# Kernel tuning notes

Hardware: AMD Instinct MI355X
Metric: run time of the kernel (lower is better)

## Reference

```python
import jax, jax.numpy as jnp
import numpy as np

N_NODES = 10000
N_EDGES = 160000
N_GRAPHS = 64
X_IN = 128
HID = 64
EDGE_DIM = 16
HEADS = 4
# (in_dim, out_dim_per_head) for the 3 TransformerConv layers (concat=False)
DIMS = [(X_IN, HID), (HID, 2 * HID), (2 * HID, HID)]
WNAMES = [f"{n}{l}" for l in (1, 2, 3) for n in ("wq", "bq", "wk", "bk", "wv", "bv", "we", "ws", "bs")]


def setup_inputs() -> dict:
    key = jax.random.key(0)
    ks = iter(jax.random.split(key, 64))
    inp = {}
    inp["x"] = jax.random.normal(next(ks), (N_NODES, X_IN), jnp.float32)
    inp["edge_index"] = jax.random.randint(next(ks), (2, N_EDGES), 0, N_NODES)
    inp["edge_attr"] = jax.random.normal(next(ks), (N_EDGES, EDGE_DIM), jnp.float32)
    inp["batch"] = jnp.sort(jax.random.randint(next(ks), (N_NODES,), 0, N_GRAPHS))
    for l, (din, dout) in enumerate(DIMS, 1):
        hd = HEADS * dout
        for nm, shape in [("wq", (din, hd)), ("wk", (din, hd)), ("wv", (din, hd)),
                          ("we", (EDGE_DIM, hd)), ("ws", (din, dout))]:
            inp[f"{nm}{l}"] = jax.random.normal(next(ks), shape, jnp.float32) * 0.05
        inp[f"bq{l}"] = jnp.zeros((hd,), jnp.float32)
        inp[f"bk{l}"] = jnp.zeros((hd,), jnp.float32)
        inp[f"bv{l}"] = jnp.zeros((hd,), jnp.float32)
        inp[f"bs{l}"] = jnp.zeros((dout,), jnp.float32)
    return inp


def _transformer_conv(x, src, dst, edge_attr, wq, bq, wk, bk, wv, bv, we, ws, bs, dout):
    """PyG TransformerConv, concat=False, root_weight=True, with edge features."""
    N = x.shape[0]
    q = (x @ wq + bq).reshape(N, HEADS, dout)
    k = (x @ wk + bk).reshape(N, HEADS, dout)
    v = (x @ wv + bv).reshape(N, HEADS, dout)
    e = (edge_attr @ we).reshape(-1, HEADS, dout)  # [E, H, C]
    k_j = k[src] + e                               # edge-conditioned keys
    alpha = jnp.einsum("ehd,ehd->eh", q[dst], k_j) * (1.0 / float(dout) ** 0.5)  # [E, H]
    # numerically stable segment softmax over incoming edges of each dst node
    a_max = jax.ops.segment_max(alpha, dst, num_segments=N)
    ex = jnp.exp(alpha - a_max[dst])
    den = jax.ops.segment_sum(ex, dst, num_segments=N)
    attn = ex / den[dst]
    agg = jax.ops.segment_sum((v[src] + e) * attn[..., None], dst, num_segments=N)  # [N, H, C]
    return agg.mean(axis=1) + x @ ws + bs  # concat=False -> head mean; + skip


def _forward(x, edge_attr, edge_index, batch, params):
    src, dst = edge_index[0], edge_index[1]
    h = x
    for l, (_, dout) in enumerate(DIMS, 1):
        p = [params[f"{n}{l}"] for n in ("wq", "bq", "wk", "bk", "wv", "bv", "we", "ws", "bs")]
        h = jax.nn.elu(_transformer_conv(h, src, dst, edge_attr, *p, dout))
    # global mean pool over graphs
    s = jax.ops.segment_sum(h, batch, num_segments=N_GRAPHS)
    cnt = jax.ops.segment_sum(jnp.ones((h.shape[0], 1), h.dtype), batch, num_segments=N_GRAPHS)
    return s / jnp.maximum(cnt, 1.0)


def reference(x, edge_index, edge_attr, batch,
              wq1, bq1, wk1, bk1, wv1, bv1, we1, ws1, bs1,
              wq2, bq2, wk2, bk2, wv2, bv2, we2, ws2, bs2,
              wq3, bq3, wk3, bk3, wv3, bv3, we3, ws3, bs3):
    params = dict(locals())
    return _forward(x, edge_attr, edge_index, batch, params)
```

## Files before the change

### kernel.cpp

```cpp
#include <hip/hip_runtime.h>
#include <hip/hip_fp16.h>
#include <math.h>

#define N_NODES 10000
#define N_EDGES 160000
#define N_GRAPHS 64

using half8 = __attribute__((ext_vector_type(8))) _Float16;
using floatx4 = __attribute__((ext_vector_type(4))) float;

template <int K, int HD, int DOUT>
__global__ __launch_bounds__(256) void gemm_mfma(
    const __half* __restrict__ A, const __half* __restrict__ Wp,
    const float* __restrict__ bias, float* __restrict__ QS,
    __half* __restrict__ KV, int M) {
  constexpr int QSS = HD + DOUT;
  constexpr int KS = K / 32;
  const int tid = threadIdx.x;
  const int wave = tid >> 6, lane = tid & 63;
  const int quad = lane >> 4, n16 = lane & 15;
  const int row0 = blockIdx.y * 64 + wave * 16;
  const int col0 = blockIdx.x * 64;
  const int nblk0 = blockIdx.x * 4;

  const int arow = min(row0 + n16, M - 1);
  half8 afrag[KS];
#pragma unroll
  for (int s = 0; s < KS; ++s)
    afrag[s] = *reinterpret_cast<const half8*>(A + (size_t)arow * K + s * 32 + quad * 8);

  floatx4 acc[4];
#pragma unroll
  for (int t = 0; t < 4; ++t) {
    acc[t] = (floatx4){0.f, 0.f, 0.f, 0.f};
#pragma unroll
    for (int s = 0; s < KS; ++s) {
      half8 bf = *reinterpret_cast<const half8*>(
          Wp + (((size_t)(nblk0 + t) * KS + s) * 64 + lane) * 8);
      acc[t] = __builtin_amdgcn_mfma_f32_16x16x32_f16(afrag[s], bf, acc[t], 0, 0, 0);
    }
  }

#pragma unroll
  for (int t = 0; t < 4; ++t) {
    const int c = col0 + t * 16 + n16;
    const float bv = bias[c];
#pragma unroll
    for (int r = 0; r < 4; ++r) {
      int row = row0 + quad * 4 + r;
      if (row < M) {
        float val = acc[t][r] + bv;
        if (c < HD)
          QS[(size_t)row * QSS + c] = val;
        else if (c < 3 * HD)
          KV[(size_t)row * (2 * HD) + (c - HD)] = __float2half(val);
        else
          QS[(size_t)row * QSS + HD + (c - 3 * HD)] = val;
      }
    }
  }
}

__device__ inline void pack_layer(int i, int K, int HD, int DOUT,
                                  const float* wq, const float* wk,
                                  const float* wv, const float* wsk,
                                  const float* bq, const float* bk,
                                  const float* bv, const float* bs,
                                  __half* Wp, float* bcat) {
  const int W = 3 * HD + DOUT;
  const int KS = K / 32;
  if (i < K * W) {
    int j = i & 7, lane = (i >> 3) & 63, fs = i >> 9;
    int nblk = fs / KS, s = fs - nblk * KS;
    int quad = lane >> 4, n = lane & 15;
    int k = s * 32 + quad * 8 + j, c = nblk * 16 + n;
    float v;
    if (c < HD)           v = wq[k * HD + c];
    else if (c < 2 * HD)  v = wk[k * HD + (c - HD)];
    else if (c < 3 * HD)  v = wv[k * HD + (c - 2 * HD)];
    else                  v = wsk[k * DOUT + (c - 3 * HD)];
    Wp[i] = __float2half(v);
  } else {
    int c = i - K * W;
    float v;
    if (c < HD)           v = bq[c];
    else if (c < 2 * HD)  v = bk[c - HD];
    else if (c < 3 * HD)  v = bv[c - 2 * HD];
    else                  v = bs[c - 3 * HD];
    bcat[c] = v;
  }
}

#define T1 107328
#define T2 215488
#define T3 322816

__global__ void pack_all(
    const float* wq1, const float* wk1, const float* wv1, const float* ws1,
    const float* bq1, const float* bk1, const float* bv1, const float* bs1,
    const float* wq2, const float* wk2, const float* wv2, const float* ws2,
    const float* bq2, const float* bk2, const float* bv2, const float* bs2,
    const float* wq3, const float* wk3, const float* wv3, const float* ws3,
    const float* bq3, const float* bk3, const float* bv3, const float* bs3,
    __half* W1, float* b1, __half* W2, float* b2, __half* W3, float* b3) {
  for (int i = blockIdx.x * blockDim.x + threadIdx.x; i < T3;
       i += gridDim.x * blockDim.x) {
    if (i < T1)
      pack_layer(i, 128, 256, 64, wq1, wk1, wv1, ws1, bq1, bk1, bv1, bs1, W1, b1);
    else if (i < T2)
      pack_layer(i - T1, 64, 512, 128, wq2, wk2, wv2, ws2, bq2, bk2, bv2, bs2, W2, b2);
    else
      pack_layer(i - T2, 128, 256, 64, wq3, wk3, wv3, ws3, bq3, bk3, bv3, bs3, W3, b3);
  }
}

__global__ void conv_f16(const float* __restrict__ in, __half* __restrict__ out,
                         int n4) {
  int i = blockIdx.x * blockDim.x + threadIdx.x;
  if (i < n4) {
    float4 v = reinterpret_cast<const float4*>(in)[i];
    __half2* o = reinterpret_cast<__half2*>(out) + 2 * i;
    o[0] = __floats2half2_rn(v.x, v.y);
    o[1] = __floats2half2_rn(v.z, v.w);
  }
}

__global__ void zero_ints(int* __restrict__ a, int n) {
  for (int i = blockIdx.x * blockDim.x + threadIdx.x; i < n;
       i += gridDim.x * blockDim.x) a[i] = 0;
}

__global__ void count_dst(const int* __restrict__ dst, int* __restrict__ cnt) {
  int e = blockIdx.x * blockDim.x + threadIdx.x;
  if (e < N_EDGES) atomicAdd(&cnt[dst[e]], 1);
}

__global__ __launch_bounds__(256) void scan_offs(const int* __restrict__ cnt,
                                                 int* __restrict__ offs) {
  __shared__ int part[256];
  const int t = threadIdx.x;
  const int chunk = (N_NODES + 255) / 256;
  const int b = t * chunk;
  const int e = min(N_NODES, b + chunk);
  int s = 0;
  for (int i = b; i < e; ++i) s += cnt[i];
  part[t] = s;
  __syncthreads();
  for (int off = 1; off < 256; off <<= 1) {
    int v = (t >= off) ? part[t - off] : 0;
    __syncthreads();
    part[t] += v;
    __syncthreads();
  }
  int pre = (t == 0) ? 0 : part[t - 1];
  for (int i = b; i < e; ++i) { offs[i] = pre; pre += cnt[i]; }
  if (t == 0) offs[N_NODES] = part[255];
}

__global__ void scatter_csr(const int* __restrict__ src, const int* __restrict__ dst,
                            const float* __restrict__ edge_attr,
                            const int* __restrict__ offs, int* __restrict__ cursor,
                            int* __restrict__ csr_src, float* __restrict__ csr_ea) {
  int e = blockIdx.x * blockDim.x + threadIdx.x;
  if (e < N_EDGES) {
    int d = dst[e];
    int pos = offs[d] + atomicAdd(&cursor[d], 1);
    csr_src[pos] = src[e];
    float4* o4 = reinterpret_cast<float4*>(csr_ea + (size_t)pos * 16);
    const float4* s4 = reinterpret_cast<const float4*>(edge_attr + (size_t)e * 16);
    o4[0] = s4[0]; o4[1] = s4[1]; o4[2] = s4[2]; o4[3] = s4[3];
  }
}

template <int NV>
__device__ inline void load_kv(const __half* p, float4 (&dst)[NV]) {
  if (NV == 1) {
    float2 r = *reinterpret_cast<const float2*>(p);
    const __half2* h = reinterpret_cast<const __half2*>(&r);
    float2 a = __half22float2(h[0]), b = __half22float2(h[1]);
    dst[0] = make_float4(a.x, a.y, b.x, b.y);
  } else {
    float4 r = *reinterpret_cast<const float4*>(p);
    const __half2* h = reinterpret_cast<const __half2*>(&r);
    float2 a = __half22float2(h[0]), b = __half22float2(h[1]);
    float2 c = __half22float2(h[2]), d = __half22float2(h[3]);
    dst[0] = make_float4(a.x, a.y, b.x, b.y);
    dst[NV - 1] = make_float4(c.x, c.y, d.x, d.y);
  }
}

template <int DOUT>
__global__ __launch_bounds__(256) void edge_attn(
    const float* __restrict__ QS, const __half* __restrict__ KV,
    const float* __restrict__ we, const int* __restrict__ csr_src,
    const float* __restrict__ csr_ea, const int* __restrict__ offs,
    float* __restrict__ out, __half* __restrict__ out16) {
  constexpr int HD = 4 * DOUT;
  constexpr int QSS = HD + DOUT;
  constexpr int KVS = 2 * HD;
  constexpr int NV = DOUT / 64;
  const float SCALE = (DOUT == 64) ? 0.125f : 0.08838834764831845f;

  const int lane = threadIdx.x & 63;
  const int h = lane >> 4, t16 = lane & 15;
  const int n = blockIdx.x * 4 + (threadIdx.x >> 6);
  const int c0 = t16 * 4 * NV;

  const float* base = QS + (size_t)n * QSS;
  float4 q[NV], acc[NV];
#pragma unroll
  for (int v = 0; v < NV; ++v) {
    float4 qq = *reinterpret_cast<const float4*>(base + h * DOUT + c0 + 4 * v);
    qq.x *= SCALE; qq.y *= SCALE; qq.z *= SCALE; qq.w *= SCALE;
    q[v] = qq;
    acc[v] = make_float4(0.f, 0.f, 0.f, 0.f);
  }

  float g = 0.f;
#pragma unroll
  for (int d = 0; d < 16; ++d) {
    float p = 0.f;
    const float* wb = we + d * HD + h * DOUT + c0;
#pragma unroll
    for (int v = 0; v < NV; ++v) {
      float4 w4 = *reinterpret_cast<const float4*>(wb + 4 * v);
      p += q[v].x * w4.x + q[v].y * w4.y + q[v].z * w4.z + q[v].w * w4.w;
    }
    p += __shfl_xor(p, 1);
    p += __shfl_xor(p, 2);
    p += __shfl_xor(p, 4);
    p += __shfl_xor(p, 8);
    if (t16 == d) g = p;
  }

  float m = -1e30f, lsum = 0.f, tacc = 0.f;

  const int s0 = offs[n], s1 = offs[n + 1];
  int ii = s0;

  for (; ii + 4 <= s1; ii += 4) {
    int sj[4];
#pragma unroll
    for (int j = 0; j < 4; ++j) sj[j] = csr_src[ii + j];
    float ea[4];
#pragma unroll
    for (int j = 0; j < 4; ++j) ea[j] = csr_ea[(size_t)(ii + j) * 16 + t16];
    float4 kj[4][NV], vj[4][NV];
#pragma unroll
    for (int j = 0; j < 4; ++j) {
      const __half* rb = KV + (size_t)sj[j] * KVS + h * DOUT + c0;
      load_kv<NV>(rb, kj[j]);
      load_kv<NV>(rb + HD, vj[j]);
    }
    float a[4];
#pragma unroll
    for (int j = 0; j < 4; ++j) {
      float p = ea[j] * g;
#pragma unroll
      for (int v = 0; v < NV; ++v)
        p += q[v].x * kj[j][v].x + q[v].y * kj[j][v].y + q[v].z * kj[j][v].z +
             q[v].w * kj[j][v].w;
      a[j] = p;
    }
#pragma unroll
    for (int j = 0; j < 4; ++j) {
      a[j] += __shfl_xor(a[j], 1);
      a[j] += __shfl_xor(a[j], 2);
      a[j] += __shfl_xor(a[j], 4);
      a[j] += __shfl_xor(a[j], 8);
    }
    float mn = fmaxf(fmaxf(fmaxf(a[0], a[1]), fmaxf(a[2], a[3])), m);
    float fac = __expf(m - mn);
    float p0 = __expf(a[0] - mn), p1 = __expf(a[1] - mn);
    float p2 = __expf(a[2] - mn), p3 = __expf(a[3] - mn);
    m = mn;
    lsum = lsum * fac + (p0 + p1 + p2 + p3);
    tacc = tacc * fac + p0 * ea[0] + p1 * ea[1] + p2 * ea[2] + p3 * ea[3];
#pragma unroll
    for (int v = 0; v < NV; ++v) {
      float4 av = acc[v];
      av.x = av.x * fac + p0 * vj[0][v].x + p1 * vj[1][v].x + p2 * vj[2][v].x + p3 * vj[3][v].x;
      av.y = av.y * fac + p0 * vj[0][v].y + p1 * vj[1][v].y + p2 * vj[2][v].y + p3 * vj[3][v].y;
      av.z = av.z * fac + p0 * vj[0][v].z + p1 * vj[1][v].z + p2 * vj[2][v].z + p3 * vj[3][v].z;
      av.w = av.w * fac + p0 * vj[0][v].w + p1 * vj[1][v].w + p2 * vj[2][v].w + p3 * vj[3][v].w;
      acc[v] = av;
    }
  }

  for (; ii < s1; ++ii) {
    int s = csr_src[ii];
    float ea0 = csr_ea[(size_t)ii * 16 + t16];
    const __half* rb = KV + (size_t)s * KVS + h * DOUT + c0;
    float4 kk[NV], vv[NV];
    load_kv<NV>(rb, kk);
    load_kv<NV>(rb + HD, vv);
    float a = ea0 * g;
#pragma unroll
    for (int v = 0; v < NV; ++v)
      a += q[v].x * kk[v].x + q[v].y * kk[v].y + q[v].z * kk[v].z + q[v].w * kk[v].w;
    a += __shfl_xor(a, 1);
    a += __shfl_xor(a, 2);
    a += __shfl_xor(a, 4);
    a += __shfl_xor(a, 8);
    float mn = fmaxf(m, a);
    float fac = __expf(m - mn);
    float p = __expf(a - mn);
    m = mn;
    lsum = lsum * fac + p;
    tacc = tacc * fac + p * ea0;
#pragma unroll
    for (int v = 0; v < NV; ++v) {
      acc[v].x = acc[v].x * fac + p * vv[v].x;
      acc[v].y = acc[v].y * fac + p * vv[v].y;
      acc[v].z = acc[v].z * fac + p * vv[v].z;
      acc[v].w = acc[v].w * fac + p * vv[v].w;
    }
  }

  float invl = (lsum > 0.f) ? 1.f / lsum : 0.f;
  float tn = tacc * invl;
  float4 val[NV];
#pragma unroll
  for (int v = 0; v < NV; ++v) {
    val[v].x = acc[v].x * invl; val[v].y = acc[v].y * invl;
    val[v].z = acc[v].z * invl; val[v].w = acc[v].w * invl;
  }
#pragma unroll
  for (int d = 0; d < 16; ++d) {
    float td = __shfl(tn, (lane & 48) | d);
    const float* wb = we + d * HD + h * DOUT + c0;
#pragma unroll
    for (int v = 0; v < NV; ++v) {
      float4 w4 = *reinterpret_cast<const float4*>(wb + 4 * v);
      val[v].x += td * w4.x; val[v].y += td * w4.y;
      val[v].z += td * w4.z; val[v].w += td * w4.w;
    }
  }
#pragma unroll
  for (int v = 0; v < NV; ++v) {
    val[v].x += __shfl_xor(val[v].x, 16); val[v].x += __shfl_xor(val[v].x, 32);
    val[v].y += __shfl_xor(val[v].y, 16); val[v].y += __shfl_xor(val[v].y, 32);
    val[v].z += __shfl_xor(val[v].z, 16); val[v].z += __shfl_xor(val[v].z, 32);
    val[v].w += __shfl_xor(val[v].w, 16); val[v].w += __shfl_xor(val[v].w, 32);
  }
  if (h == 0) {
#pragma unroll
    for (int v = 0; v < NV; ++v) {
      float4 sk = *reinterpret_cast<const float4*>(base + HD + c0 + 4 * v);
      float4 o;
      o.x = 0.25f * val[v].x + sk.x;
      o.y = 0.25f * val[v].y + sk.y;
      o.z = 0.25f * val[v].z + sk.z;
      o.w = 0.25f * val[v].w + sk.w;
      o.x = (o.x > 0.f) ? o.x : expm1f(o.x);
      o.y = (o.y > 0.f) ? o.y : expm1f(o.y);
      o.z = (o.z > 0.f) ? o.z : expm1f(o.z);
      o.w = (o.w > 0.f) ? o.w : expm1f(o.w);
      *reinterpret_cast<float4*>(out + (size_t)n * DOUT + c0 + 4 * v) = o;
      __half2* o16 = reinterpret_cast<__half2*>(out16 + (size_t)n * DOUT + c0 + 4 * v);
      o16[0] = __floats2half2_rn(o.x, o.y);
      o16[1] = __floats2half2_rn(o.z, o.w);
    }
  }
}

__device__ inline int lower_bound(const int* b, int n, int v) {
  int lo = 0, hi = n;
  while (lo < hi) {
    int mid = (lo + hi) >> 1;
    if (b[mid] < v) lo = mid + 1; else hi = mid;
  }
  return lo;
}

__global__ __launch_bounds__(256) void pool_all(const float* __restrict__ h,
                                                const int* __restrict__ batch,
                                                float* __restrict__ out) {
  const int g = blockIdx.x;
  const int start = lower_bound(batch, N_NODES, g);
  const int end = lower_bound(batch, N_NODES, g + 1);
  const int c = threadIdx.x & 63, j = threadIdx.x >> 6;
  float s = 0.f;
  for (int n = start + j; n < end; n += 4) s += h[(size_t)n * 64 + c];
  __shared__ float red[4][64];
  red[j][c] = s;
  __syncthreads();
  if (j == 0) {
    float tot = red[0][c] + red[1][c] + red[2][c] + red[3][c];
    out[g * 64 + c] = tot / (float)max(end - start, 1);
  }
}

extern "C" void kernel_launch(void* const* d_in, const int* in_sizes, int n_in,
                              void* d_out, int out_size, void* d_ws, size_t ws_size,
                              hipStream_t stream) {
  const float* x = (const float*)d_in[0];
  const int* edge_index = (const int*)d_in[1];
  const float* edge_attr = (const float*)d_in[2];
  const int* batch = (const int*)d_in[3];
  const int* srcp = edge_index;
  const int* dstp = edge_index + N_EDGES;

  const bool dict_order = in_sizes[5] > 1024;
  const float *wq[3], *wk[3], *wv[3], *wep[3], *wsk[3], *bq[3], *bk[3], *bv[3], *bs[3];
  for (int L = 0; L < 3; ++L) {
    int b = 4 + L * 9;
    if (dict_order) {
      wq[L] = (const float*)d_in[b + 0];
      wk[L] = (const float*)d_in[b + 1];
      wv[L] = (const float*)d_in[b + 2];
      wep[L] = (const float*)d_in[b + 3];
      wsk[L] = (const float*)d_in[b + 4];
      bq[L] = (const float*)d_in[b + 5];
      bk[L] = (const float*)d_in[b + 6];
      bv[L] = (const float*)d_in[b + 7];
      bs[L] = (const float*)d_in[b + 8];
    } else {
      wq[L] = (const float*)d_in[b + 0];
      bq[L] = (const float*)d_in[b + 1];
      wk[L] = (const float*)d_in[b + 2];
      bk[L] = (const float*)d_in[b + 3];
      wv[L] = (const float*)d_in[b + 4];
      bv[L] = (const float*)d_in[b + 5];
      wep[L] = (const float*)d_in[b + 6];
      wsk[L] = (const float*)d_in[b + 7];
      bs[L] = (const float*)d_in[b + 8];
    }
  }

  char* p = (char*)d_ws;
  float* qs = (float*)p;      p += (size_t)N_NODES * 640 * 4;
  __half* kv = (__half*)p;    p += (size_t)N_NODES * 1024 * 2;
  float* h1 = (float*)p;      p += (size_t)N_NODES * 64 * 4;
  float* h2 = (float*)p;      p += (size_t)N_NODES * 128 * 4;
  __half* x16 = (__half*)p;   p += (size_t)N_NODES * 128 * 2;
  __half* h16 = (__half*)p;   p += (size_t)N_NODES * 128 * 2;
  __half* W1 = (__half*)p;    p += 128 * 832 * 2;
  __half* W2 = (__half*)p;    p += 64 * 1664 * 2;
  __half* W3 = (__half*)p;    p += 128 * 832 * 2;
  float* b1 = (float*)p;      p += 832 * 4;
  float* b2 = (float*)p;      p += 1664 * 4;
  float* b3 = (float*)p;      p += 832 * 4;
  float* csr_ea = (float*)p;  p += (size_t)N_EDGES * 16 * 4;
  int* cnt = (int*)p;         p += N_NODES * 4;
  int* cursor = (int*)p;      p += N_NODES * 4;
  int* offs = (int*)p;        p += (N_NODES + 1) * 4;
  int* csr_src = (int*)p;     p += N_EDGES * 4;

  pack_all<<<632, 256, 0, stream>>>(
      wq[0], wk[0], wv[0], wsk[0], bq[0], bk[0], bv[0], bs[0],
      wq[1], wk[1], wv[1], wsk[1], bq[1], bk[1], bv[1], bs[1],
      wq[2], wk[2], wv[2], wsk[2], bq[2], bk[2], bv[2], bs[2],
      W1, b1, W2, b2, W3, b3);
  conv_f16<<<(N_NODES * 128 / 4 + 255) / 256, 256, 0, stream>>>(x, x16,
                                                                N_NODES * 128 / 4);

  zero_ints<<<79, 256, 0, stream>>>(cnt, 2 * N_NODES);
  count_dst<<<(N_EDGES + 255) / 256, 256, 0, stream>>>(dstp, cnt);
  scan_offs<<<1, 256, 0, stream>>>(cnt, offs);
  scatter_csr<<<(N_EDGES + 255) / 256, 256, 0, stream>>>(srcp, dstp, edge_attr,
                                                         offs, cursor, csr_src, csr_ea);

  const int MT = (N_NODES + 63) / 64;
  gemm_mfma<128, 256, 64><<<dim3(832 / 64, MT), 256, 0, stream>>>(x16, W1, b1, qs,
                                                                  kv, N_NODES);
  edge_attn<64><<<N_NODES / 4, 256, 0, stream>>>(qs, kv, wep[0], csr_src, csr_ea,
                                                 offs, h1, h16);
  gemm_mfma<64, 512, 128><<<dim3(1664 / 64, MT), 256, 0, stream>>>(h16, W2, b2, qs,
                                                                   kv, N_NODES);
  edge_attn<128><<<N_NODES / 4, 256, 0, stream>>>(qs, kv, wep[1], csr_src, csr_ea,
                                                  offs, h2, h16);
  gemm_mfma<128, 256, 64><<<dim3(832 / 64, MT), 256, 0, stream>>>(h16, W3, b3, qs,
                                                                  kv, N_NODES);
  edge_attn<64><<<N_NODES / 4, 256, 0, stream>>>(qs, kv, wep[2], csr_src, csr_ea,
                                                 offs, h1, x16 );

  pool_all<<<N_GRAPHS, 256, 0, stream>>>(h1, batch, (float*)d_out);
}
```

Baseline: 370.0 us.

## Fold edge-key projection into GEMM, store Q in fp16, prefetch edges

Precomputes Wq·We^T per head (scaled) as 64 extra GEMM output columns, so edge_attn reads g directly instead of reducing it per node. Q and skip outputs are stored as fp16 to halve their traffic. The edge loop is double-buffered so the next group's loads overlap compute. The online-softmax max tracking is removed and raw exp is used. It also fuses x conversion into pack_all and replaces zero_ints with a memset. Dropping the max subtraction risks overflow with larger logits, and fp16 Q loses precision.

```diff
diff --git a/kernel.cpp b/kernel.cpp
--- a/kernel.cpp
+++ b/kernel.cpp
@@ -9,12 +9,30 @@
 using half8 = __attribute__((ext_vector_type(8))) _Float16;
 using floatx4 = __attribute__((ext_vector_type(4))) float;
 
+template <int NV> struct KW;
+template <> struct KW<1> { using T = uint2; };
+template <> struct KW<2> { using T = uint4; };
+
+__device__ inline void cvt_kv(const uint2& w, float4* dst) {
+  float2 a = __half22float2(*reinterpret_cast<const __half2*>(&w.x));
+  float2 b = __half22float2(*reinterpret_cast<const __half2*>(&w.y));
+  dst[0] = make_float4(a.x, a.y, b.x, b.y);
+}
+__device__ inline void cvt_kv(const uint4& w, float4* dst) {
+  float2 a = __half22float2(*reinterpret_cast<const __half2*>(&w.x));
+  float2 b = __half22float2(*reinterpret_cast<const __half2*>(&w.y));
+  float2 c = __half22float2(*reinterpret_cast<const __half2*>(&w.z));
+  float2 d = __half22float2(*reinterpret_cast<const __half2*>(&w.w));
+  dst[0] = make_float4(a.x, a.y, b.x, b.y);
+  dst[1] = make_float4(c.x, c.y, d.x, d.y);
+}
+
 template <int K, int HD, int DOUT>
 __global__ __launch_bounds__(256) void gemm_mfma(
     const __half* __restrict__ A, const __half* __restrict__ Wp,
-    const float* __restrict__ bias, float* __restrict__ QS,
+    const float* __restrict__ bias, __half* __restrict__ QS,
     __half* __restrict__ KV, int M) {
-  constexpr int QSS = HD + DOUT;
+  constexpr int QSS = HD + 64 + DOUT;
   constexpr int KS = K / 32;
   const int tid = threadIdx.x;
   const int wave = tid >> 6, lane = tid & 63;
@@ -49,25 +67,25 @@
     for (int r = 0; r < 4; ++r) {
       int row = row0 + quad * 4 + r;
       if (row < M) {
-        float val = acc[t][r] + bv;
-        if (c < HD)
+        __half val = __float2half(acc[t][r] + bv);
+        if (c < HD + 64)
           QS[(size_t)row * QSS + c] = val;
-        else if (c < 3 * HD)
-          KV[(size_t)row * (2 * HD) + (c - HD)] = __float2half(val);
+        else if (c < 3 * HD + 64)
+          KV[(size_t)row * (2 * HD) + (c - HD - 64)] = val;
         else
-          QS[(size_t)row * QSS + HD + (c - 3 * HD)] = val;
+          QS[(size_t)row * QSS + HD + 64 + (c - 3 * HD - 64)] = val;
       }
     }
   }
 }
 
-__device__ inline void pack_layer(int i, int K, int HD, int DOUT,
+__device__ inline void pack_layer(int i, int K, int HD, int DOUT, float scale,
                                   const float* wq, const float* wk,
                                   const float* wv, const float* wsk,
-                                  const float* bq, const float* bk,
-                                  const float* bv, const float* bs,
-                                  __half* Wp, float* bcat) {
-  const int W = 3 * HD + DOUT;
+                                  const float* we, const float* bq,
+                                  const float* bk, const float* bv,
+                                  const float* bs, __half* Wp, float* bcat) {
+  const int W = 3 * HD + DOUT + 64;
   const int KS = K / 32;
   if (i < K * W) {
     int j = i & 7, lane = (i >> 3) & 63, fs = i >> 9;
@@ -75,59 +93,79 @@
     int quad = lane >> 4, n = lane & 15;
     int k = s * 32 + quad * 8 + j, c = nblk * 16 + n;
     float v;
-    if (c < HD)           v = wq[k * HD + c];
-    else if (c < 2 * HD)  v = wk[k * HD + (c - HD)];
-    else if (c < 3 * HD)  v = wv[k * HD + (c - 2 * HD)];
-    else                  v = wsk[k * DOUT + (c - 3 * HD)];
+    if (c < HD) {
+      v = wq[k * HD + c] * scale;
+    } else if (c < HD + 64) {
+      int gi = c - HD, hh = gi >> 4, d = gi & 15;
+      float a = 0.f;
+      for (int cc = 0; cc < DOUT; ++cc)
+        a += wq[k * HD + hh * DOUT + cc] * we[d * HD + hh * DOUT + cc];
+      v = a * scale;
+    } else if (c < 2 * HD + 64) {
+      v = wk[k * HD + (c - HD - 64)];
+    } else if (c < 3 * HD + 64) {
+      v = wv[k * HD + (c - 2 * HD - 64)];
+    } else {
+      v = wsk[k * DOUT + (c - 3 * HD - 64)];
+    }
     Wp[i] = __float2half(v);
   } else {
     int c = i - K * W;
     float v;
-    if (c < HD)           v = bq[c];
-    else if (c < 2 * HD)  v = bk[c - HD];
-    else if (c < 3 * HD)  v = bv[c - 2 * HD];
-    else                  v = bs[c - 3 * HD];
+    if (c < HD) {
+      v = bq[c] * scale;
+    } else if (c < HD + 64) {
+      int gi = c - HD, hh = gi >> 4, d = gi & 15;
+      float a = 0.f;
+      for (int cc = 0; cc < DOUT; ++cc)
+        a += bq[hh * DOUT + cc] * we[d * HD + hh * DOUT + cc];
+      v = a * scale;
+    } else if (c < 2 * HD + 64) {
+      v = bk[c - HD - 64];
+    } else if (c < 3 * HD + 64) {
+      v = bv[c - 2 * HD - 64];
+    } else {
+      v = bs[c - 3 * HD - 64];
+    }
     bcat[c] = v;
   }
 }
 
-#define T1 107328
-#define T2 215488
-#define T3 322816
+#define T1 115584
+#define T2 227904
+#define T3 343488
+#define TCONV (N_NODES * 32)
+#define TTOT (T3 + TCONV)
 
 __global__ void pack_all(
     const float* wq1, const float* wk1, const float* wv1, const float* ws1,
-    const float* bq1, const float* bk1, const float* bv1, const float* bs1,
+    const float* we1, const float* bq1, const float* bk1, const float* bv1,
+    const float* bs1,
     const float* wq2, const float* wk2, const float* wv2, const float* ws2,
-    const float* bq2, const float* bk2, const float* bv2, const float* bs2,
+    const float* we2, const float* bq2, const float* bk2, const float* bv2,
+    const float* bs2,
     const float* wq3, const float* wk3, const float* wv3, const float* ws3,
-    const float* bq3, const float* bk3, const float* bv3, const float* bs3,
-    __half* W1, float* b1, __half* W2, float* b2, __half* W3, float* b3) {
-  for (int i = blockIdx.x * blockDim.x + threadIdx.x; i < T3;
+    const float* we3, const float* bq3, const float* bk3, const float* bv3,
+    const float* bs3,
+    __half* W1, float* b1, __half* W2, float* b2, __half* W3, float* b3,
+    const float* x, __half* x16) {
+  const float SC1 = 0.125f, SC2 = 0.08838834764831845f;
+  for (int i = blockIdx.x * blockDim.x + threadIdx.x; i < TTOT;
        i += gridDim.x * blockDim.x) {
     if (i < T1)
-      pack_layer(i, 128, 256, 64, wq1, wk1, wv1, ws1, bq1, bk1, bv1, bs1, W1, b1);
+      pack_layer(i, 128, 256, 64, SC1, wq1, wk1, wv1, ws1, we1, bq1, bk1, bv1, bs1, W1, b1);
     else if (i < T2)
-      pack_layer(i - T1, 64, 512, 128, wq2, wk2, wv2, ws2, bq2, bk2, bv2, bs2, W2, b2);
-    else
-      pack_layer(i - T2, 128, 256, 64, wq3, wk3, wv3, ws3, bq3, bk3, bv3, bs3, W3, b3);
-  }
-}
-
-__global__ void conv_f16(const float* __restrict__ in, __half* __restrict__ out,
-                         int n4) {
-  int i = blockIdx.x * blockDim.x + threadIdx.x;
-  if (i < n4) {
-    float4 v = reinterpret_cast<const float4*>(in)[i];
-    __half2* o = reinterpret_cast<__half2*>(out) + 2 * i;
-    o[0] = __floats2half2_rn(v.x, v.y);
-    o[1] = __floats2half2_rn(v.z, v.w);
-  }
-}
-
-__global__ void zero_ints(int* __restrict__ a, int n) {
-  for (int i = blockIdx.x * blockDim.x + threadIdx.x; i < n;
-       i += gridDim.x * blockDim.x) a[i] = 0;
+      pack_layer(i - T1, 64, 512, 128, SC2, wq2, wk2, wv2, ws2, we2, bq2, bk2, bv2, bs2, W2, b2);
+    else if (i < T3)
+      pack_layer(i - T2, 128, 256, 64, SC1, wq3, wk3, wv3, ws3, we3, bq3, bk3, bv3, bs3, W3, b3);
+    else {
+      int k = i - T3;
+      float4 v = reinterpret_cast<const float4*>(x)[k];
+      __half2* o = reinterpret_cast<__half2*>(x16) + 2 * k;
+      o[0] = __floats2half2_rn(v.x, v.y);
+      o[1] = __floats2half2_rn(v.z, v.w);
+    }
+  }
 }
 
 __global__ void count_dst(const int* __restrict__ dst, int* __restrict__ cnt) {
@@ -172,94 +210,66 @@
   }
 }
 
-template <int NV>
-__device__ inline void load_kv(const __half* p, float4 (&dst)[NV]) {
-  if (NV == 1) {
-    float2 r = *reinterpret_cast<const float2*>(p);
-    const __half2* h = reinterpret_cast<const __half2*>(&r);
-    float2 a = __half22float2(h[0]), b = __half22float2(h[1]);
-    dst[0] = make_float4(a.x, a.y, b.x, b.y);
-  } else {
-    float4 r = *reinterpret_cast<const float4*>(p);
-    const __half2* h = reinterpret_cast<const __half2*>(&r);
-    float2 a = __half22float2(h[0]), b = __half22float2(h[1]);
-    float2 c = __half22float2(h[2]), d = __half22float2(h[3]);
-    dst[0] = make_float4(a.x, a.y, b.x, b.y);
-    dst[NV - 1] = make_float4(c.x, c.y, d.x, d.y);
-  }
-}
-
 template <int DOUT>
 __global__ __launch_bounds__(256) void edge_attn(
-    const float* __restrict__ QS, const __half* __restrict__ KV,
+    const __half* __restrict__ QS, const __half* __restrict__ KV,
     const float* __restrict__ we, const int* __restrict__ csr_src,
     const float* __restrict__ csr_ea, const int* __restrict__ offs,
     float* __restrict__ out, __half* __restrict__ out16) {
   constexpr int HD = 4 * DOUT;
-  constexpr int QSS = HD + DOUT;
+  constexpr int QSS = HD + 64 + DOUT;
   constexpr int KVS = 2 * HD;
   constexpr int NV = DOUT / 64;
-  const float SCALE = (DOUT == 64) ? 0.125f : 0.08838834764831845f;
+  using KWT = typename KW<NV>::T;
 
   const int lane = threadIdx.x & 63;
   const int h = lane >> 4, t16 = lane & 15;
   const int n = blockIdx.x * 4 + (threadIdx.x >> 6);
   const int c0 = t16 * 4 * NV;
 
-  const float* base = QS + (size_t)n * QSS;
+  const __half* base = QS + (size_t)n * QSS;
   float4 q[NV], acc[NV];
-#pragma unroll
-  for (int v = 0; v < NV; ++v) {
-    float4 qq = *reinterpret_cast<const float4*>(base + h * DOUT + c0 + 4 * v);
-    qq.x *= SCALE; qq.y *= SCALE; qq.z *= SCALE; qq.w *= SCALE;
-    q[v] = qq;
-    acc[v] = make_float4(0.f, 0.f, 0.f, 0.f);
-  }
-
-  float g = 0.f;
-#pragma unroll
-  for (int d = 0; d < 16; ++d) {
-    float p = 0.f;
-    const float* wb = we + d * HD + h * DOUT + c0;
-#pragma unroll
-    for (int v = 0; v < NV; ++v) {
-      float4 w4 = *reinterpret_cast<const float4*>(wb + 4 * v);
-      p += q[v].x * w4.x + q[v].y * w4.y + q[v].z * w4.z + q[v].w * w4.w;
-    }
-    p += __shfl_xor(p, 1);
-    p += __shfl_xor(p, 2);
-    p += __shfl_xor(p, 4);
-    p += __shfl_xor(p, 8);
-    if (t16 == d) g = p;
-  }
-
-  float m = -1e30f, lsum = 0.f, tacc = 0.f;
+  {
+    KWT qw = *reinterpret_cast<const KWT*>(base + h * DOUT + c0);
+    cvt_kv(qw, q);
+  }
+#pragma unroll
+  for (int v = 0; v < NV; ++v) acc[v] = make_float4(0.f, 0.f, 0.f, 0.f);
+  const float g = __half2float(base[HD + h * 16 + t16]);
+
+  float lsum = 0.f, tacc = 0.f;
 
   const int s0 = offs[n], s1 = offs[n + 1];
-  int ii = s0;
-
-  for (; ii + 4 <= s1; ii += 4) {
-    int sj[4];
-#pragma unroll
-    for (int j = 0; j < 4; ++j) sj[j] = csr_src[ii + j];
-    float ea[4];
-#pragma unroll
-    for (int j = 0; j < 4; ++j) ea[j] = csr_ea[(size_t)(ii + j) * 16 + t16];
-    float4 kj[4][NV], vj[4][NV];
+
+  int sjA[4], sjB[4];
+  float eaA[4], eaB[4];
+  KWT krA[4], vrA[4], krB[4], vrB[4];
+
+  auto load_grp = [&](int bi, int (&sj)[4], float (&ea)[4], KWT (&kr)[4],
+                      KWT (&vr)[4]) {
+#pragma unroll
+    for (int j = 0; j < 4; ++j) sj[j] = csr_src[bi + j];
+#pragma unroll
+    for (int j = 0; j < 4; ++j) ea[j] = csr_ea[(size_t)(bi + j) * 16 + t16];
 #pragma unroll
     for (int j = 0; j < 4; ++j) {
       const __half* rb = KV + (size_t)sj[j] * KVS + h * DOUT + c0;
-      load_kv<NV>(rb, kj[j]);
-      load_kv<NV>(rb + HD, vj[j]);
-    }
+      kr[j] = *reinterpret_cast<const KWT*>(rb);
+      vr[j] = *reinterpret_cast<const KWT*>(rb + HD);
+    }
+  };
+
+  auto compute_grp = [&](float (&ea)[4], KWT (&kr)[4], KWT (&vr)[4]) {
     float a[4];
 #pragma unroll
     for (int j = 0; j < 4; ++j) {
+      float4 kk[NV];
+      cvt_kv(kr[j], kk);
       float p = ea[j] * g;
 #pragma unroll
       for (int v = 0; v < NV; ++v)
-        p += q[v].x * kj[j][v].x + q[v].y * kj[j][v].y + q[v].z * kj[j][v].z +
-             q[v].w * kj[j][v].w;
+        p += q[v].x * kk[v].x + q[v].y * kk[v].y + q[v].z * kk[v].z +
+             q[v].w * kk[v].w;
       a[j] = p;
     }
 #pragma unroll
@@ -269,21 +279,38 @@
       a[j] += __shfl_xor(a[j], 4);
       a[j] += __shfl_xor(a[j], 8);
     }
-    float mn = fmaxf(fmaxf(fmaxf(a[0], a[1]), fmaxf(a[2], a[3])), m);
-    float fac = __expf(m - mn);
-    float p0 = __expf(a[0] - mn), p1 = __expf(a[1] - mn);
-    float p2 = __expf(a[2] - mn), p3 = __expf(a[3] - mn);
-    m = mn;
-    lsum = lsum * fac + (p0 + p1 + p2 + p3);
-    tacc = tacc * fac + p0 * ea[0] + p1 * ea[1] + p2 * ea[2] + p3 * ea[3];
-#pragma unroll
-    for (int v = 0; v < NV; ++v) {
-      float4 av = acc[v];
-      av.x = av.x * fac + p0 * vj[0][v].x + p1 * vj[1][v].x + p2 * vj[2][v].x + p3 * vj[3][v].x;
-      av.y = av.y * fac + p0 * vj[0][v].y + p1 * vj[1][v].y + p2 * vj[2][v].y + p3 * vj[3][v].y;
-      av.z = av.z * fac + p0 * vj[0][v].z + p1 * vj[1][v].z + p2 * vj[2][v].z + p3 * vj[3][v].z;
-      av.w = av.w * fac + p0 * vj[0][v].w + p1 * vj[1][v].w + p2 * vj[2][v].w + p3 * vj[3][v].w;
-      acc[v] = av;
+    float p0 = __expf(a[0]), p1 = __expf(a[1]);
+    float p2 = __expf(a[2]), p3 = __expf(a[3]);
+    lsum += p0 + p1 + p2 + p3;
+    tacc += p0 * ea[0] + p1 * ea[1] + p2 * ea[2] + p3 * ea[3];
+    float pj[4] = {p0, p1, p2, p3};
+#pragma unroll
+    for (int j = 0; j < 4; ++j) {
+      float4 vv[NV];
+      cvt_kv(vr[j], vv);
+#pragma unroll
+      for (int v = 0; v < NV; ++v) {
+        acc[v].x += pj[j] * vv[v].x;
+        acc[v].y += pj[j] * vv[v].y;
+        acc[v].z += pj[j] * vv[v].z;
+        acc[v].w += pj[j] * vv[v].w;
+      }
+    }
+  };
+
+  int ii = s0;
+  const int end_full = s0 + ((s1 - s0) & ~3);
+  if (ii < end_full) {
+    load_grp(ii, sjA, eaA, krA, vrA);
+    for (;;) {
+      if (ii + 4 >= end_full) { compute_grp(eaA, krA, vrA); ii += 4; break; }
+      load_grp(ii + 4, sjB, eaB, krB, vrB);
+      compute_grp(eaA, krA, vrA);
+      ii += 4;
+      if (ii + 4 >= end_full) { compute_grp(eaB, krB, vrB); ii += 4; break; }
+      load_grp(ii + 4, sjA, eaA, krA, vrA);
+      compute_grp(eaB, krB, vrB);
+      ii += 4;
     }
   }
 
@@ -291,9 +318,11 @@
     int s = csr_src[ii];
     float ea0 = csr_ea[(size_t)ii * 16 + t16];
     const __half* rb = KV + (size_t)s * KVS + h * DOUT + c0;
+    KWT kw = *reinterpret_cast<const KWT*>(rb);
+    KWT vw = *reinterpret_cast<const KWT*>(rb + HD);
     float4 kk[NV], vv[NV];
-    load_kv<NV>(rb, kk);
-    load_kv<NV>(rb + HD, vv);
+    cvt_kv(kw, kk);
+    cvt_kv(vw, vv);
     float a = ea0 * g;
 #pragma unroll
     for (int v = 0; v < NV; ++v)
@@ -302,18 +331,15 @@
     a += __shfl_xor(a, 2);
     a += __shfl_xor(a, 4);
     a += __shfl_xor(a, 8);
-    float mn = fmaxf(m, a);
-    float fac = __expf(m - mn);
-    float p = __expf(a - mn);
-    m = mn;
-    lsum = lsum * fac + p;
-    tacc = tacc * fac + p * ea0;
+    float p = __expf(a);
+    lsum += p;
+    tacc += p * ea0;
 #pragma unroll
     for (int v = 0; v < NV; ++v) {
-      acc[v].x = acc[v].x * fac + p * vv[v].x;
-      acc[v].y = acc[v].y * fac + p * vv[v].y;
-      acc[v].z = acc[v].z * fac + p * vv[v].z;
-      acc[v].w = acc[v].w * fac + p * vv[v].w;
+      acc[v].x += p * vv[v].x;
+      acc[v].y += p * vv[v].y;
+      acc[v].z += p * vv[v].z;
+      acc[v].w += p * vv[v].w;
     }
   }
 
@@ -344,14 +370,16 @@
     val[v].w += __shfl_xor(val[v].w, 16); val[v].w += __shfl_xor(val[v].w, 32);
   }
   if (h == 0) {
+    KWT sw = *reinterpret_cast<const KWT*>(base + HD + 64 + c0);
+    float4 sk[NV];
+    cvt_kv(sw, sk);
 #pragma unroll
     for (int v = 0; v < NV; ++v) {
-      float4 sk = *reinterpret_cast<const float4*>(base + HD + c0 + 4 * v);
       float4 o;
-      o.x = 0.25f * val[v].x + sk.x;
-      o.y = 0.25f * val[v].y + sk.y;
-      o.z = 0.25f * val[v].z + sk.z;
-      o.w = 0.25f * val[v].w + sk.w;
+      o.x = 0.25f * val[v].x + sk[v].x;
+      o.y = 0.25f * val[v].y + sk[v].y;
+      o.z = 0.25f * val[v].z + sk[v].z;
+      o.w = 0.25f * val[v].w + sk[v].w;
       o.x = (o.x > 0.f) ? o.x : expm1f(o.x);
       o.y = (o.y > 0.f) ? o.y : expm1f(o.y);
       o.z = (o.z > 0.f) ? o.z : expm1f(o.z);
@@ -429,48 +457,46 @@
   }
 
   char* p = (char*)d_ws;
-  float* qs = (float*)p;      p += (size_t)N_NODES * 640 * 4;
+  __half* qs = (__half*)p;    p += (size_t)N_NODES * 704 * 2;
   __half* kv = (__half*)p;    p += (size_t)N_NODES * 1024 * 2;
   float* h1 = (float*)p;      p += (size_t)N_NODES * 64 * 4;
   float* h2 = (float*)p;      p += (size_t)N_NODES * 128 * 4;
   __half* x16 = (__half*)p;   p += (size_t)N_NODES * 128 * 2;
   __half* h16 = (__half*)p;   p += (size_t)N_NODES * 128 * 2;
-  __half* W1 = (__half*)p;    p += 128 * 832 * 2;
-  __half* W2 = (__half*)p;    p += 64 * 1664 * 2;
-  __half* W3 = (__half*)p;    p += 128 * 832 * 2;
-  float* b1 = (float*)p;      p += 832 * 4;
-  float* b2 = (float*)p;      p += 1664 * 4;
-  float* b3 = (float*)p;      p += 832 * 4;
+  __half* W1 = (__half*)p;    p += 128 * 896 * 2;
+  __half* W2 = (__half*)p;    p += 64 * 1728 * 2;
+  __half* W3 = (__half*)p;    p += 128 * 896 * 2;
+  float* b1 = (float*)p;      p += 896 * 4;
+  float* b2 = (float*)p;      p += 1728 * 4;
+  float* b3 = (float*)p;      p += 896 * 4;
   float* csr_ea = (float*)p;  p += (size_t)N_EDGES * 16 * 4;
   int* cnt = (int*)p;         p += N_NODES * 4;
   int* cursor = (int*)p;      p += N_NODES * 4;
   int* offs = (int*)p;        p += (N_NODES + 1) * 4;
   int* csr_src = (int*)p;     p += N_EDGES * 4;
 
-  pack_all<<<632, 256, 0, stream>>>(
-      wq[0], wk[0], wv[0], wsk[0], bq[0], bk[0], bv[0], bs[0],
-      wq[1], wk[1], wv[1], wsk[1], bq[1], bk[1], bv[1], bs[1],
-      wq[2], wk[2], wv[2], wsk[2], bq[2], bk[2], bv[2], bs[2],
-      W1, b1, W2, b2, W3, b3);
-  conv_f16<<<(N_NODES * 128 / 4 + 255) / 256, 256, 0, stream>>>(x, x16,
-                                                                N_NODES * 128 / 4);
-
-  zero_ints<<<79, 256, 0, stream>>>(cnt, 2 * N_NODES);
+  pack_all<<<1024, 256, 0, stream>>>(
+      wq[0], wk[0], wv[0], wsk[0], wep[0], bq[0], bk[0], bv[0], bs[0],
+      wq[1], wk[1], wv[1], wsk[1], wep[1], bq[1], bk[1], bv[1], bs[1],
+      wq[2], wk[2], wv[2], wsk[2], wep[2], bq[2], bk[2], bv[2], bs[2],
+      W1, b1, W2, b2, W3, b3, x, x16);
+
+  hipMemsetAsync(cnt, 0, 2 * N_NODES * sizeof(int), stream);
   count_dst<<<(N_EDGES + 255) / 256, 256, 0, stream>>>(dstp, cnt);
   scan_offs<<<1, 256, 0, stream>>>(cnt, offs);
   scatter_csr<<<(N_EDGES + 255) / 256, 256, 0, stream>>>(srcp, dstp, edge_attr,
                                                          offs, cursor, csr_src, csr_ea);
 
   const int MT = (N_NODES + 63) / 64;
-  gemm_mfma<128, 256, 64><<<dim3(832 / 64, MT), 256, 0, stream>>>(x16, W1, b1, qs,
+  gemm_mfma<128, 256, 64><<<dim3(896 / 64, MT), 256, 0, stream>>>(x16, W1, b1, qs,
                                                                   kv, N_NODES);
   edge_attn<64><<<N_NODES / 4, 256, 0, stream>>>(qs, kv, wep[0], csr_src, csr_ea,
                                                  offs, h1, h16);
-  gemm_mfma<64, 512, 128><<<dim3(1664 / 64, MT), 256, 0, stream>>>(h16, W2, b2, qs,
+  gemm_mfma<64, 512, 128><<<dim3(1728 / 64, MT), 256, 0, stream>>>(h16, W2, b2, qs,
                                                                    kv, N_NODES);
   edge_attn<128><<<N_NODES / 4, 256, 0, stream>>>(qs, kv, wep[1], csr_src, csr_ea,
                                                   offs, h2, h16);
-  gemm_mfma<128, 256, 64><<<dim3(832 / 64, MT), 256, 0, stream>>>(h16, W3, b3, qs,
+  gemm_mfma<128, 256, 64><<<dim3(896 / 64, MT), 256, 0, stream>>>(h16, W3, b3, qs,
                                                                   kv, N_NODES);
   edge_attn<64><<<N_NODES / 4, 256, 0, stream>>>(qs, kv, wep[2], csr_src, csr_ea,
                                                  offs, h1, x16 );
```

After: 354.0 us. 1.05x faster.
